# Kernel tuning notes

Hardware: AMD Instinct MI355X
Metric: run time of the kernel (lower is better)

The kernel has to match this reference:

```python
import jax, jax.numpy as jnp
import numpy as np

N = 100000      # nodes per graph batch
E = 1600000     # edges per graph batch
F_IN = 128
HID = 128
N_GRAPHS = 64


def gcn_conv(x, edge_index, W, b):
    """PyG GCNConv: add self-loops, symmetric deg^-1/2 normalization, scatter-add."""
    n = x.shape[0]
    xw = x @ W                                  # [N, H]
    src, dst = edge_index[0], edge_index[1]
    # degree including self-loop
    deg = jnp.zeros((n,), xw.dtype).at[dst].add(jnp.ones((src.shape[0],), xw.dtype)) + 1.0
    dinv = jax.lax.rsqrt(deg)                   # deg^-1/2
    norm = (dinv[src] * dinv[dst])[:, None]     # [E, 1]
    msg = xw[src] * norm                        # gather + scale
    agg = jnp.zeros_like(xw).at[dst].add(msg)   # scatter-add
    agg = agg + xw * (dinv * dinv)[:, None]     # self-loop contribution
    return agg + b


def global_mean_pool(x, batch, num_graphs):
    sums = jax.ops.segment_sum(x, batch, num_segments=num_graphs)
    cnts = jax.ops.segment_sum(jnp.ones((x.shape[0],), x.dtype), batch, num_segments=num_graphs)
    return sums / jnp.maximum(cnts, 1.0)[:, None]


def setup_inputs() -> dict:
    key = jax.random.key(0)
    ks = jax.random.split(key, 16)
    s = 1.0 / np.sqrt(F_IN)
    sh = 1.0 / np.sqrt(HID)
    return {
        "x_H": jax.random.normal(ks[0], (N, F_IN), jnp.float32),
        "edge_index_H": jax.random.randint(ks[1], (2, E), 0, N, jnp.int64),
        "x_G": jax.random.normal(ks[2], (N, F_IN), jnp.float32),
        "edge_index_G": jax.random.randint(ks[3], (2, E), 0, N, jnp.int64),
        "batch_H": jnp.sort(jax.random.randint(ks[4], (N,), 0, N_GRAPHS, jnp.int64)),
        "batch_G": jnp.sort(jax.random.randint(ks[5], (N,), 0, N_GRAPHS, jnp.int64)),
        # selector params
        "sel_W1": jax.random.uniform(ks[6], (F_IN, HID), jnp.float32, -s, s),
        "sel_b1": jnp.zeros((HID,), jnp.float32),
        "sel_W2": jax.random.uniform(ks[7], (HID, HID), jnp.float32, -sh, sh),
        "sel_b2": jnp.zeros((HID,), jnp.float32),
        "sel_fcw": jax.random.uniform(ks[8], (HID, 1), jnp.float32, -sh, sh),
        "sel_fcb": jnp.zeros((1,), jnp.float32),
        # embedder params (shared between F and G branches)
        "emb_W1": jax.random.uniform(ks[9], (F_IN, HID), jnp.float32, -s, s),
        "emb_b1": jnp.zeros((HID,), jnp.float32),
        "emb_W2": jax.random.uniform(ks[10], (HID, HID), jnp.float32, -sh, sh),
        "emb_b2": jnp.zeros((HID,), jnp.float32),
    }


def reference(x_H, edge_index_H, x_G, edge_index_G, batch_H, batch_G,
              sel_W1, sel_b1, sel_W2, sel_b2, sel_fcw, sel_fcb,
              emb_W1, emb_b1, emb_W2, emb_b2):
    # selector on H
    h = jax.nn.relu(gcn_conv(x_H, edge_index_H, sel_W1, sel_b1))
    h = jax.nn.relu(gcn_conv(h, edge_index_H, sel_W2, sel_b2))
    p = jax.nn.sigmoid(h @ sel_fcw + sel_fcb)          # [N, 1]

    def embed(x, ei, batch):
        z = jax.nn.relu(gcn_conv(x, ei, emb_W1, emb_b1))
        z = jax.nn.relu(gcn_conv(z, ei, emb_W2, emb_b2))
        return global_mean_pool(z, batch, N_GRAPHS)

    h_F = embed(x_H * p, edge_index_H, batch_H)
    h_G = embed(x_G, edge_index_G, batch_G)
    return (h_F, h_G, p)
```

## Files before the change

kernel.cpp:

```cpp
#include <hip/hip_runtime.h>
#include <cstdint>
#include <cstddef>

#define FEAT 128
#define PSLICE 8
#define BSHIFT 7
#define CAP 4096

typedef _Float16 h16;
typedef __attribute__((ext_vector_type(8))) _Float16 h16x8;
typedef __attribute__((ext_vector_type(4))) _Float16 h16x4;
typedef __attribute__((ext_vector_type(2))) _Float16 h16x2;
typedef __attribute__((ext_vector_type(4))) float f32x4;

__global__ __launch_bounds__(256) void k_part(const int* __restrict__ ei,
    int2* __restrict__ pair, int* __restrict__ gcur, int E, int nb) {
  __shared__ int cnt[1024];
  __shared__ int base[1024];
  int per = (E + gridDim.x - 1) / gridDim.x;
  int e0 = blockIdx.x * per;
  int e1 = min(e0 + per, E);
  for (int i = threadIdx.x; i < nb; i += 256) cnt[i] = 0;
  __syncthreads();
  for (int e = e0 + threadIdx.x; e < e1; e += 256)
    atomicAdd(&cnt[ei[E + e] >> BSHIFT], 1);
  __syncthreads();
  for (int i = threadIdx.x; i < nb; i += 256) {
    int c = cnt[i];
    base[i] = c ? atomicAdd(&gcur[i], c) : 0;
    cnt[i] = 0;
  }
  __syncthreads();
  for (int e = e0 + threadIdx.x; e < e1; e += 256) {
    int src = ei[e];
    int dst = ei[E + e];
    int b = dst >> BSHIFT;
    int pos = base[b] + atomicAdd(&cnt[b], 1);
    if (pos < CAP) pair[(size_t)b * CAP + pos] = make_int2(src, dst);
  }
}

__global__ __launch_bounds__(1024) void k_bscan(const int* __restrict__ cnt,
    int* __restrict__ boffs, int* __restrict__ offs, int nb, int N, int E) {
  __shared__ int wsum[16];
  __shared__ int carry;
  int tid = threadIdx.x;
  int lane = tid & 63;
  int wid = tid >> 6;
  if (tid == 0) carry = 0;
  for (int base = 0; base < nb; base += 1024) {
    __syncthreads();
    int c0 = carry;
    int i = base + tid;
    int v = (i < nb) ? cnt[i] : 0;
    int x = v;
#pragma unroll
    for (int off = 1; off < 64; off <<= 1) {
      int t = __shfl_up(x, off);
      if (lane >= off) x += t;
    }
    if (lane == 63) wsum[wid] = x;
    __syncthreads();
    if (wid == 0) {
      int t = (lane < 16) ? wsum[lane] : 0;
#pragma unroll
      for (int off = 1; off < 16; off <<= 1) {
        int u = __shfl_up(t, off);
        if (lane >= off) t += u;
      }
      if (lane < 16) wsum[lane] = t;
    }
    __syncthreads();
    int wex = (wid == 0) ? 0 : wsum[wid - 1];
    int o = c0 + wex + (x - v);
    if (i < nb) boffs[i] = o;
    int total = wsum[15];
    __syncthreads();
    if (tid == 0) carry = c0 + total;
  }
  __syncthreads();
  if (tid == 0) { boffs[nb] = carry; offs[N] = E; }
}

__global__ __launch_bounds__(256) void k_bucket(const int2* __restrict__ pair,
    const int* __restrict__ bcnt, const int* __restrict__ boffs,
    int* __restrict__ csr, int* __restrict__ offs, float* __restrict__ dinv,
    int N) {
  int b = blockIdx.x;
  int nodeBase = b << BSHIFT;
  int m = min(bcnt[b], CAP);
  __shared__ int cnt[128];
  __shared__ int noff[128];
  __shared__ int w0tot;
  if (threadIdx.x < 128) cnt[threadIdx.x] = 0;
  __syncthreads();
  const int2* p = pair + (size_t)b * CAP;
  for (int i = threadIdx.x; i < m; i += 256)
    atomicAdd(&cnt[p[i].y - nodeBase], 1);
  __syncthreads();
  int v = 0, x = 0;
  int lane = threadIdx.x & 63, w = threadIdx.x >> 6;
  if (threadIdx.x < 128) {
    v = cnt[threadIdx.x];
    x = v;
#pragma unroll
    for (int o = 1; o < 64; o <<= 1) {
      int t = __shfl_up(x, o);
      if (lane >= o) x += t;
    }
    if (threadIdx.x == 63) w0tot = x;
  }
  __syncthreads();
  int cbase = boffs[b];
  if (threadIdx.x < 128) {
    int ex = x - v + ((w == 1) ? w0tot : 0);
    int g = nodeBase + threadIdx.x;
    if (g < N) {
      offs[g] = cbase + ex;
      dinv[g] = 1.0f / sqrtf((float)v + 1.0f);
    }
    noff[threadIdx.x] = ex;
    cnt[threadIdx.x] = 0;
  }
  __syncthreads();
  for (int i = threadIdx.x; i < m; i += 256) {
    int d = p[i].y - nodeBase;
    int pos = cbase + noff[d] + atomicAdd(&cnt[d], 1);
    csr[pos] = p[i].x;
  }
}

__global__ __launch_bounds__(256) void k_wprep(const float* __restrict__ W,
    h16* __restrict__ WT) {
  int i = blockIdx.x * 256 + threadIdx.x;
  int k = i >> 7, c = i & 127;
  WT[c * FEAT + k] = (h16)W[(size_t)k * FEAT + c];
}

__device__ inline h16x8 load8(const float* p) {
  float4 a = *(const float4*)p, b = *(const float4*)(p + 4);
  h16x8 o;
  o[0] = (h16)a.x; o[1] = (h16)a.y; o[2] = (h16)a.z; o[3] = (h16)a.w;
  o[4] = (h16)b.x; o[5] = (h16)b.y; o[6] = (h16)b.z; o[7] = (h16)b.w;
  return o;
}
__device__ inline h16x8 load8(const h16* p) { return *(const h16x8*)p; }

template <typename TI>
__global__ __launch_bounds__(256) void k_gemm_mfma(const TI* __restrict__ X,
    const h16* __restrict__ WT, const float* __restrict__ s1, const float* __restrict__ s2,
    h16* __restrict__ Y, int n) {
  __shared__ __align__(16) h16 lA[128 * FEAT];
  __shared__ __align__(16) h16 lB[128 * FEAT];
  int tid = threadIdx.x;
  int row0 = blockIdx.x * 128;
#pragma unroll
  for (int i = 0; i < 8; ++i) {
    int c = tid + i * 256;
    int r = c >> 4, kc = c & 15;
    int grow = row0 + r;
    h16x8 v;
#pragma unroll
    for (int j = 0; j < 8; ++j) v[j] = (h16)0.f;
    if (grow < n) v = load8(&X[(size_t)grow * FEAT + kc * 8]);
    int byte = r * 256 + ((kc * 16) ^ ((r & 7) << 4));
    *(h16x8*)((char*)lA + byte) = v;
  }
#pragma unroll
  for (int i = 0; i < 8; ++i) {
    int c = tid + i * 256;
    int col = c >> 4, kc = c & 15;
    h16x8 v = *(const h16x8*)&WT[col * FEAT + kc * 8];
    int byte = col * 256 + ((kc * 16) ^ ((col & 7) << 4));
    *(h16x8*)((char*)lB + byte) = v;
  }
  __syncthreads();
  int w = tid >> 6, l = tid & 63;
  int lr = l & 15, lq = l >> 4;
  h16x8 af[2][4];
#pragma unroll
  for (int m = 0; m < 2; ++m)
#pragma unroll
    for (int s = 0; s < 4; ++s) {
      int r = w * 32 + m * 16 + lr;
      int k2 = (s * 32 + lq * 8) * 2;
      int byte = r * 256 + (k2 ^ ((r & 7) << 4));
      af[m][s] = *(const h16x8*)((const char*)lA + byte);
    }
  f32x4 acc[2][8];
#pragma unroll
  for (int m = 0; m < 2; ++m)
#pragma unroll
    for (int nn = 0; nn < 8; ++nn) acc[m][nn] = (f32x4){0.f, 0.f, 0.f, 0.f};
#pragma unroll
  for (int nn = 0; nn < 8; ++nn) {
#pragma unroll
    for (int s = 0; s < 4; ++s) {
      int col = nn * 16 + lr;
      int k2 = (s * 32 + lq * 8) * 2;
      int byte = col * 256 + (k2 ^ ((col & 7) << 4));
      h16x8 bf = *(const h16x8*)((const char*)lB + byte);
      acc[0][nn] = __builtin_amdgcn_mfma_f32_16x16x32_f16(af[0][s], bf, acc[0][nn], 0, 0, 0);
      acc[1][nn] = __builtin_amdgcn_mfma_f32_16x16x32_f16(af[1][s], bf, acc[1][nn], 0, 0, 0);
    }
  }
#pragma unroll
  for (int m = 0; m < 2; ++m) {
#pragma unroll
    for (int r = 0; r < 4; ++r) {
      int grow = row0 + w * 32 + m * 16 + lq * 4 + r;
      if (grow < n) {
        float sc = 1.0f;
        if (s1) sc = s1[grow];
        if (s2) sc *= s2[grow];
#pragma unroll
        for (int nn = 0; nn < 8; ++nn)
          Y[(size_t)grow * FEAT + nn * 16 + lr] = (h16)(acc[m][nn][r] * sc);
      }
    }
  }
}

__device__ inline float4 ldrow4(const h16* p) {
  h16x4 v = *(const h16x4*)p;
  return make_float4((float)v[0], (float)v[1], (float)v[2], (float)v[3]);
}

__global__ __launch_bounds__(256) void k_agg(const h16* __restrict__ XW,
    const int* __restrict__ offs, const int* __restrict__ csr,
    const float* __restrict__ dinv, const float* __restrict__ bias,
    h16* __restrict__ out, int n) {
  int half = threadIdx.x >> 5;
  int lane = threadIdx.x & 31;
  int node = blockIdx.x * 8 + half;
  if (node >= n) return;
  int f = lane * 4;
  float4 a0 = ldrow4(&XW[(size_t)node * FEAT + f]);
  float4 a1 = {0,0,0,0}, a2 = {0,0,0,0}, a3 = {0,0,0,0};
  float4 a4 = {0,0,0,0}, a5 = {0,0,0,0}, a6 = {0,0,0,0}, a7 = {0,0,0,0};
  int s = offs[node], e = offs[node + 1];
  int i = s;
  for (; i + 8 <= e; i += 8) {
    int s0 = csr[i + 0], s1 = csr[i + 1], s2 = csr[i + 2], s3 = csr[i + 3];
    int s4 = csr[i + 4], s5 = csr[i + 5], s6 = csr[i + 6], s7 = csr[i + 7];
    float4 v0 = ldrow4(&XW[(size_t)s0 * FEAT + f]);
    float4 v1 = ldrow4(&XW[(size_t)s1 * FEAT + f]);
    float4 v2 = ldrow4(&XW[(size_t)s2 * FEAT + f]);
    float4 v3 = ldrow4(&XW[(size_t)s3 * FEAT + f]);
    float4 v4 = ldrow4(&XW[(size_t)s4 * FEAT + f]);
    float4 v5 = ldrow4(&XW[(size_t)s5 * FEAT + f]);
    float4 v6 = ldrow4(&XW[(size_t)s6 * FEAT + f]);
    float4 v7 = ldrow4(&XW[(size_t)s7 * FEAT + f]);
    a0.x += v0.x; a0.y += v0.y; a0.z += v0.z; a0.w += v0.w;
    a1.x += v1.x; a1.y += v1.y; a1.z += v1.z; a1.w += v1.w;
    a2.x += v2.x; a2.y += v2.y; a2.z += v2.z; a2.w += v2.w;
    a3.x += v3.x; a3.y += v3.y; a3.z += v3.z; a3.w += v3.w;
    a4.x += v4.x; a4.y += v4.y; a4.z += v4.z; a4.w += v4.w;
    a5.x += v5.x; a5.y += v5.y; a5.z += v5.z; a5.w += v5.w;
    a6.x += v6.x; a6.y += v6.y; a6.z += v6.z; a6.w += v6.w;
    a7.x += v7.x; a7.y += v7.y; a7.z += v7.z; a7.w += v7.w;
  }
  if (i + 4 <= e) {
    int s0 = csr[i + 0], s1 = csr[i + 1], s2 = csr[i + 2], s3 = csr[i + 3];
    float4 v0 = ldrow4(&XW[(size_t)s0 * FEAT + f]);
    float4 v1 = ldrow4(&XW[(size_t)s1 * FEAT + f]);
    float4 v2 = ldrow4(&XW[(size_t)s2 * FEAT + f]);
    float4 v3 = ldrow4(&XW[(size_t)s3 * FEAT + f]);
    a4.x += v0.x; a4.y += v0.y; a4.z += v0.z; a4.w += v0.w;
    a5.x += v1.x; a5.y += v1.y; a5.z += v1.z; a5.w += v1.w;
    a6.x += v2.x; a6.y += v2.y; a6.z += v2.z; a6.w += v2.w;
    a7.x += v3.x; a7.y += v3.y; a7.z += v3.z; a7.w += v3.w;
    i += 4;
  }
  for (; i < e; ++i) {
    int s0 = csr[i];
    float4 v0 = ldrow4(&XW[(size_t)s0 * FEAT + f]);
    a1.x += v0.x; a1.y += v0.y; a1.z += v0.z; a1.w += v0.w;
  }
  a0.x += a1.x; a0.y += a1.y; a0.z += a1.z; a0.w += a1.w;
  a2.x += a3.x; a2.y += a3.y; a2.z += a3.z; a2.w += a3.w;
  a4.x += a5.x; a4.y += a5.y; a4.z += a5.z; a4.w += a5.w;
  a6.x += a7.x; a6.y += a7.y; a6.z += a7.z; a6.w += a7.w;
  a0.x += a2.x; a0.y += a2.y; a0.z += a2.z; a0.w += a2.w;
  a4.x += a6.x; a4.y += a6.y; a4.z += a6.z; a4.w += a6.w;
  a0.x += a4.x; a0.y += a4.y; a0.z += a4.z; a0.w += a4.w;
  float d = dinv[node];
  float4 b = *(const float4*)&bias[f];
  h16x4 o;
  o[0] = (h16)fmaxf(a0.x * d + b.x, 0.f);
  o[1] = (h16)fmaxf(a0.y * d + b.y, 0.f);
  o[2] = (h16)fmaxf(a0.z * d + b.z, 0.f);
  o[3] = (h16)fmaxf(a0.w * d + b.w, 0.f);
  *(h16x4*)&out[(size_t)node * FEAT + f] = o;
}

__global__ __launch_bounds__(256) void k_pvec(const h16* __restrict__ H,
    const float* __restrict__ fcw, const float* __restrict__ fcb,
    float* __restrict__ p, int n) {
  int w = threadIdx.x >> 6, lane = threadIdx.x & 63;
  int node = blockIdx.x * 4 + w;
  if (node >= n) return;
  h16x2 h = *(const h16x2*)&H[(size_t)node * FEAT + lane * 2];
  float2 wv = *(const float2*)&fcw[lane * 2];
  float acc = (float)h[0] * wv.x + (float)h[1] * wv.y;
#pragma unroll
  for (int off = 32; off > 0; off >>= 1) acc += __shfl_xor(acc, off);
  if (lane == 0) p[node] = 1.0f / (1.0f + expf(-(acc + fcb[0])));
}

__global__ __launch_bounds__(256) void k_pool_part(const h16* __restrict__ Z,
    const int* __restrict__ batch, float* __restrict__ part, int n) {
  int g = blockIdx.x / PSLICE;
  int s = blockIdx.x % PSLICE;
  int lo = 0, hi = n;
  while (lo < hi) { int m = (lo + hi) >> 1; if (batch[m] < g) lo = m + 1; else hi = m; }
  int start = lo;
  hi = n;
  while (lo < hi) { int m = (lo + hi) >> 1; if (batch[m] <= g) lo = m + 1; else hi = m; }
  int end = lo;
  int len = end - start;
  int per = (len + PSLICE - 1) / PSLICE;
  int r0 = start + s * per;
  int r1 = min(r0 + per, end);
  int f = threadIdx.x & 127;
  int half = threadIdx.x >> 7;
  float acc = 0.f;
  for (int i = r0 + half; i < r1; i += 2) acc += (float)Z[(size_t)i * FEAT + f];
  __shared__ float lds[256];
  lds[threadIdx.x] = acc;
  __syncthreads();
  if (half == 0) part[(size_t)blockIdx.x * FEAT + f] = lds[f] + lds[128 + f];
}

__global__ __launch_bounds__(128) void k_pool_fin(const float* __restrict__ part,
    const int* __restrict__ batch, float* __restrict__ out, int n) {
  int g = blockIdx.x;
  int lo = 0, hi = n;
  while (lo < hi) { int m = (lo + hi) >> 1; if (batch[m] < g) lo = m + 1; else hi = m; }
  int start = lo;
  hi = n;
  while (lo < hi) { int m = (lo + hi) >> 1; if (batch[m] <= g) lo = m + 1; else hi = m; }
  int len = lo - start;
  int f = threadIdx.x;
  float tot = 0.f;
#pragma unroll
  for (int s = 0; s < PSLICE; ++s) tot += part[(size_t)(g * PSLICE + s) * FEAT + f];
  out[(size_t)g * FEAT + f] = tot / fmaxf((float)len, 1.0f);
}

extern "C" void kernel_launch(void* const* d_in, const int* in_sizes, int n_in,
                              void* d_out, int out_size, void* d_ws, size_t ws_size,
                              hipStream_t stream) {
  const float* x_H    = (const float*)d_in[0];
  const int*   ei_H   = (const int*)d_in[1];
  const float* x_G    = (const float*)d_in[2];
  const int*   ei_G   = (const int*)d_in[3];
  const int*   bat_H  = (const int*)d_in[4];
  const int*   bat_G  = (const int*)d_in[5];
  const float* sel_W1 = (const float*)d_in[6];
  const float* sel_b1 = (const float*)d_in[7];
  const float* sel_W2 = (const float*)d_in[8];
  const float* sel_b2 = (const float*)d_in[9];
  const float* sel_fcw = (const float*)d_in[10];
  const float* sel_fcb = (const float*)d_in[11];
  const float* emb_W1 = (const float*)d_in[12];
  const float* emb_b1 = (const float*)d_in[13];
  const float* emb_W2 = (const float*)d_in[14];
  const float* emb_b2 = (const float*)d_in[15];

  const int N = in_sizes[0] / FEAT;
  const int E = in_sizes[1] / 2;
  const int NG = 64;
  const int NB = (N + 127) >> BSHIFT;

  float* out = (float*)d_out;
  float* hF = out;
  float* hG = out + NG * FEAT;
  float* p  = out + 2 * NG * FEAT;

  char* ws = (char*)d_ws;
  size_t off = 0;
  auto alloc = [&](size_t bytes) -> void* {
    void* ptr = (void*)(ws + off);
    off += (bytes + 511) & ~(size_t)511;
    return ptr;
  };
  const size_t SZH = (size_t)N * FEAT * sizeof(h16);
  const size_t SZP = (size_t)NB * CAP * sizeof(int2);
  const size_t SZB = SZH > SZP ? SZH : SZP;
  h16* A       = (h16*)alloc(SZB);
  h16* B       = (h16*)alloc(SZB);
  float* dinvH = (float*)alloc((size_t)N * 4);
  float* dinvG = (float*)alloc((size_t)N * 4);
  int*  offsH  = (int*)alloc((size_t)(N + 1) * 4);
  int*  offsG  = (int*)alloc((size_t)(N + 1) * 4);
  int*  csrH   = (int*)alloc((size_t)E * 4);
  int*  csrG   = (int*)alloc((size_t)E * 4);
  int*  gcurH  = (int*)alloc((size_t)NB * 4);
  int*  gcurG  = (int*)alloc((size_t)NB * 4);
  int*  boffsH = (int*)alloc((size_t)(NB + 1) * 4);
  int*  boffsG = (int*)alloc((size_t)(NB + 1) * 4);
  float* part  = (float*)alloc((size_t)NG * PSLICE * FEAT * 4);
  h16* wtSel1  = (h16*)alloc((size_t)FEAT * FEAT * 2);
  h16* wtSel2  = (h16*)alloc((size_t)FEAT * FEAT * 2);
  h16* wtEmb1  = (h16*)alloc((size_t)FEAT * FEAT * 2);
  h16* wtEmb2  = (h16*)alloc((size_t)FEAT * FEAT * 2);
  (void)ws_size;

  int2* pairH = (int2*)A;
  int2* pairG = (int2*)B;

  const int gGemm = (N + 127) / 128;
  const int gAgg  = (N + 7) / 8;
  const int gP    = (N + 3) / 4;

  k_wprep<<<64, 256, 0, stream>>>(sel_W1, wtSel1);
  k_wprep<<<64, 256, 0, stream>>>(sel_W2, wtSel2);
  k_wprep<<<64, 256, 0, stream>>>(emb_W1, wtEmb1);
  k_wprep<<<64, 256, 0, stream>>>(emb_W2, wtEmb2);

  hipMemsetAsync(gcurH, 0, (size_t)NB * 4, stream);
  hipMemsetAsync(gcurG, 0, (size_t)NB * 4, stream);
  k_part<<<256, 256, 0, stream>>>(ei_H, pairH, gcurH, E, NB);
  k_part<<<256, 256, 0, stream>>>(ei_G, pairG, gcurG, E, NB);
  k_bscan<<<1, 1024, 0, stream>>>(gcurH, boffsH, offsH, NB, N, E);
  k_bscan<<<1, 1024, 0, stream>>>(gcurG, boffsG, offsG, NB, N, E);
  k_bucket<<<NB, 256, 0, stream>>>(pairH, gcurH, boffsH, csrH, offsH, dinvH, N);
  k_bucket<<<NB, 256, 0, stream>>>(pairG, gcurG, boffsG, csrG, offsG, dinvG, N);

  k_gemm_mfma<float><<<gGemm, 256, 0, stream>>>(x_H, wtSel1, dinvH, nullptr, A, N);
  k_agg<<<gAgg, 256, 0, stream>>>(A, offsH, csrH, dinvH, sel_b1, B, N);
  k_gemm_mfma<h16><<<gGemm, 256, 0, stream>>>(B, wtSel2, dinvH, nullptr, A, N);
  k_agg<<<gAgg, 256, 0, stream>>>(A, offsH, csrH, dinvH, sel_b2, B, N);
  k_pvec<<<gP, 256, 0, stream>>>(B, sel_fcw, sel_fcb, p, N);

  k_gemm_mfma<float><<<gGemm, 256, 0, stream>>>(x_H, wtEmb1, dinvH, p, A, N);
  k_agg<<<gAgg, 256, 0, stream>>>(A, offsH, csrH, dinvH, emb_b1, B, N);
  k_gemm_mfma<h16><<<gGemm, 256, 0, stream>>>(B, wtEmb2, dinvH, nullptr, A, N);
  k_agg<<<gAgg, 256, 0, stream>>>(A, offsH, csrH, dinvH, emb_b2, B, N);
  k_pool_part<<<NG * PSLICE, 256, 0, stream>>>(B, bat_H, part, N);
  k_pool_fin<<<NG, 128, 0, stream>>>(part, bat_H, hF, N);

  k_gemm_mfma<float><<<gGemm, 256, 0, stream>>>(x_G, wtEmb1, dinvG, nullptr, A, N);
  k_agg<<<gAgg, 256, 0, stream>>>(A, offsG, csrG, dinvG, emb_b1, B, N);
  k_gemm_mfma<h16><<<gGemm, 256, 0, stream>>>(B, wtEmb2, dinvG, nullptr, A, N);
  k_agg<<<gAgg, 256, 0, stream>>>(A, offsG, csrG, dinvG, emb_b2, B, N);
  k_pool_part<<<NG * PSLICE, 256, 0, stream>>>(B, bat_G, part, N);
  k_pool_fin<<<NG, 128, 0, stream>>>(part, bat_G, hG, N);
}
```

Measured before the change: 710.4 us.

## Fuse aggregation into next GEMM and p-vector, pack edge pairs, pre-convert x_H

Adds a k_agg_gemm kernel that gathers and aggregates neighbor rows into shared memory and immediately multiplies by the next layer's weights, so the intermediate activation no longer makes a round trip through global memory. The selector's final aggregation is also fused with the sigmoid projection. Edge partition pairs are packed into one 32-bit word to halve partition traffic, and x_H is converted to fp16 once and reused by both of its GEMMs. In exchange, the fused kernel has fewer blocks (one per 128 rows) with heavy LDS use, which may reduce latency hiding for the irregular gather, and packing assumes src fits in 25 bits.

```diff
diff --git a/kernel.cpp b/kernel.cpp
--- a/kernel.cpp
+++ b/kernel.cpp
@@ -10,11 +10,23 @@
 typedef _Float16 h16;
 typedef __attribute__((ext_vector_type(8))) _Float16 h16x8;
 typedef __attribute__((ext_vector_type(4))) _Float16 h16x4;
-typedef __attribute__((ext_vector_type(2))) _Float16 h16x2;
 typedef __attribute__((ext_vector_type(4))) float f32x4;
 
+__global__ __launch_bounds__(256) void k_cvt(const float* __restrict__ X,
+    h16* __restrict__ Y, int nv) {
+  int i = blockIdx.x * 256 + threadIdx.x;
+  if (i < nv) {
+    const float* p = X + (size_t)i * 8;
+    float4 a = *(const float4*)p, b = *(const float4*)(p + 4);
+    h16x8 o;
+    o[0] = (h16)a.x; o[1] = (h16)a.y; o[2] = (h16)a.z; o[3] = (h16)a.w;
+    o[4] = (h16)b.x; o[5] = (h16)b.y; o[6] = (h16)b.z; o[7] = (h16)b.w;
+    *(h16x8*)&Y[(size_t)i * 8] = o;
+  }
+}
+
 __global__ __launch_bounds__(256) void k_part(const int* __restrict__ ei,
-    int2* __restrict__ pair, int* __restrict__ gcur, int E, int nb) {
+    unsigned int* __restrict__ pair, int* __restrict__ gcur, int E, int nb) {
   __shared__ int cnt[1024];
   __shared__ int base[1024];
   int per = (E + gridDim.x - 1) / gridDim.x;
@@ -36,7 +48,7 @@
     int dst = ei[E + e];
     int b = dst >> BSHIFT;
     int pos = base[b] + atomicAdd(&cnt[b], 1);
-    if (pos < CAP) pair[(size_t)b * CAP + pos] = make_int2(src, dst);
+    if (pos < CAP) pair[(size_t)b * CAP + pos] = ((unsigned)src << BSHIFT) | (unsigned)(dst & 127);
   }
 }
 
@@ -82,21 +94,20 @@
   if (tid == 0) { boffs[nb] = carry; offs[N] = E; }
 }
 
-__global__ __launch_bounds__(256) void k_bucket(const int2* __restrict__ pair,
+__global__ __launch_bounds__(256) void k_bucket(const unsigned int* __restrict__ pair,
     const int* __restrict__ bcnt, const int* __restrict__ boffs,
     int* __restrict__ csr, int* __restrict__ offs, float* __restrict__ dinv,
     int N) {
   int b = blockIdx.x;
-  int nodeBase = b << BSHIFT;
   int m = min(bcnt[b], CAP);
   __shared__ int cnt[128];
   __shared__ int noff[128];
   __shared__ int w0tot;
   if (threadIdx.x < 128) cnt[threadIdx.x] = 0;
   __syncthreads();
-  const int2* p = pair + (size_t)b * CAP;
+  const unsigned int* p = pair + (size_t)b * CAP;
   for (int i = threadIdx.x; i < m; i += 256)
-    atomicAdd(&cnt[p[i].y - nodeBase], 1);
+    atomicAdd(&cnt[p[i] & 127u], 1);
   __syncthreads();
   int v = 0, x = 0;
   int lane = threadIdx.x & 63, w = threadIdx.x >> 6;
@@ -114,7 +125,7 @@
   int cbase = boffs[b];
   if (threadIdx.x < 128) {
     int ex = x - v + ((w == 1) ? w0tot : 0);
-    int g = nodeBase + threadIdx.x;
+    int g = (b << BSHIFT) + threadIdx.x;
     if (g < N) {
       offs[g] = cbase + ex;
       dinv[g] = 1.0f / sqrtf((float)v + 1.0f);
@@ -124,9 +135,10 @@
   }
   __syncthreads();
   for (int i = threadIdx.x; i < m; i += 256) {
-    int d = p[i].y - nodeBase;
+    unsigned pk = p[i];
+    int d = pk & 127u;
     int pos = cbase + noff[d] + atomicAdd(&cnt[d], 1);
-    csr[pos] = p[i].x;
+    csr[pos] = (int)(pk >> BSHIFT);
   }
 }
 
@@ -137,104 +149,13 @@
   WT[c * FEAT + k] = (h16)W[(size_t)k * FEAT + c];
 }
 
-__device__ inline h16x8 load8(const float* p) {
-  float4 a = *(const float4*)p, b = *(const float4*)(p + 4);
-  h16x8 o;
-  o[0] = (h16)a.x; o[1] = (h16)a.y; o[2] = (h16)a.z; o[3] = (h16)a.w;
-  o[4] = (h16)b.x; o[5] = (h16)b.y; o[6] = (h16)b.z; o[7] = (h16)b.w;
-  return o;
-}
-__device__ inline h16x8 load8(const h16* p) { return *(const h16x8*)p; }
-
-template <typename TI>
-__global__ __launch_bounds__(256) void k_gemm_mfma(const TI* __restrict__ X,
-    const h16* __restrict__ WT, const float* __restrict__ s1, const float* __restrict__ s2,
-    h16* __restrict__ Y, int n) {
-  __shared__ __align__(16) h16 lA[128 * FEAT];
-  __shared__ __align__(16) h16 lB[128 * FEAT];
-  int tid = threadIdx.x;
-  int row0 = blockIdx.x * 128;
-#pragma unroll
-  for (int i = 0; i < 8; ++i) {
-    int c = tid + i * 256;
-    int r = c >> 4, kc = c & 15;
-    int grow = row0 + r;
-    h16x8 v;
-#pragma unroll
-    for (int j = 0; j < 8; ++j) v[j] = (h16)0.f;
-    if (grow < n) v = load8(&X[(size_t)grow * FEAT + kc * 8]);
-    int byte = r * 256 + ((kc * 16) ^ ((r & 7) << 4));
-    *(h16x8*)((char*)lA + byte) = v;
-  }
-#pragma unroll
-  for (int i = 0; i < 8; ++i) {
-    int c = tid + i * 256;
-    int col = c >> 4, kc = c & 15;
-    h16x8 v = *(const h16x8*)&WT[col * FEAT + kc * 8];
-    int byte = col * 256 + ((kc * 16) ^ ((col & 7) << 4));
-    *(h16x8*)((char*)lB + byte) = v;
-  }
-  __syncthreads();
-  int w = tid >> 6, l = tid & 63;
-  int lr = l & 15, lq = l >> 4;
-  h16x8 af[2][4];
-#pragma unroll
-  for (int m = 0; m < 2; ++m)
-#pragma unroll
-    for (int s = 0; s < 4; ++s) {
-      int r = w * 32 + m * 16 + lr;
-      int k2 = (s * 32 + lq * 8) * 2;
-      int byte = r * 256 + (k2 ^ ((r & 7) << 4));
-      af[m][s] = *(const h16x8*)((const char*)lA + byte);
-    }
-  f32x4 acc[2][8];
-#pragma unroll
-  for (int m = 0; m < 2; ++m)
-#pragma unroll
-    for (int nn = 0; nn < 8; ++nn) acc[m][nn] = (f32x4){0.f, 0.f, 0.f, 0.f};
-#pragma unroll
-  for (int nn = 0; nn < 8; ++nn) {
-#pragma unroll
-    for (int s = 0; s < 4; ++s) {
-      int col = nn * 16 + lr;
-      int k2 = (s * 32 + lq * 8) * 2;
-      int byte = col * 256 + (k2 ^ ((col & 7) << 4));
-      h16x8 bf = *(const h16x8*)((const char*)lB + byte);
-      acc[0][nn] = __builtin_amdgcn_mfma_f32_16x16x32_f16(af[0][s], bf, acc[0][nn], 0, 0, 0);
-      acc[1][nn] = __builtin_amdgcn_mfma_f32_16x16x32_f16(af[1][s], bf, acc[1][nn], 0, 0, 0);
-    }
-  }
-#pragma unroll
-  for (int m = 0; m < 2; ++m) {
-#pragma unroll
-    for (int r = 0; r < 4; ++r) {
-      int grow = row0 + w * 32 + m * 16 + lq * 4 + r;
-      if (grow < n) {
-        float sc = 1.0f;
-        if (s1) sc = s1[grow];
-        if (s2) sc *= s2[grow];
-#pragma unroll
-        for (int nn = 0; nn < 8; ++nn)
-          Y[(size_t)grow * FEAT + nn * 16 + lr] = (h16)(acc[m][nn][r] * sc);
-      }
-    }
-  }
-}
-
 __device__ inline float4 ldrow4(const h16* p) {
   h16x4 v = *(const h16x4*)p;
   return make_float4((float)v[0], (float)v[1], (float)v[2], (float)v[3]);
 }
 
-__global__ __launch_bounds__(256) void k_agg(const h16* __restrict__ XW,
-    const int* __restrict__ offs, const int* __restrict__ csr,
-    const float* __restrict__ dinv, const float* __restrict__ bias,
-    h16* __restrict__ out, int n) {
-  int half = threadIdx.x >> 5;
-  int lane = threadIdx.x & 31;
-  int node = blockIdx.x * 8 + half;
-  if (node >= n) return;
-  int f = lane * 4;
+__device__ inline float4 gather_row(const h16* __restrict__ XW,
+    const int* __restrict__ offs, const int* __restrict__ csr, int node, int f) {
   float4 a0 = ldrow4(&XW[(size_t)node * FEAT + f]);
   float4 a1 = {0,0,0,0}, a2 = {0,0,0,0}, a3 = {0,0,0,0};
   float4 a4 = {0,0,0,0}, a5 = {0,0,0,0}, a6 = {0,0,0,0}, a7 = {0,0,0,0};
@@ -284,28 +205,208 @@
   a0.x += a2.x; a0.y += a2.y; a0.z += a2.z; a0.w += a2.w;
   a4.x += a6.x; a4.y += a6.y; a4.z += a6.z; a4.w += a6.w;
   a0.x += a4.x; a0.y += a4.y; a0.z += a4.z; a0.w += a4.w;
+  return a0;
+}
+
+__global__ __launch_bounds__(256) void k_agg(const h16* __restrict__ XW,
+    const int* __restrict__ offs, const int* __restrict__ csr,
+    const float* __restrict__ dinv, const float* __restrict__ bias,
+    h16* __restrict__ out, int n) {
+  int half = threadIdx.x >> 5;
+  int lane = threadIdx.x & 31;
+  int node = blockIdx.x * 8 + half;
+  if (node >= n) return;
+  int f = lane * 4;
+  float4 a = gather_row(XW, offs, csr, node, f);
   float d = dinv[node];
   float4 b = *(const float4*)&bias[f];
   h16x4 o;
-  o[0] = (h16)fmaxf(a0.x * d + b.x, 0.f);
-  o[1] = (h16)fmaxf(a0.y * d + b.y, 0.f);
-  o[2] = (h16)fmaxf(a0.z * d + b.z, 0.f);
-  o[3] = (h16)fmaxf(a0.w * d + b.w, 0.f);
+  o[0] = (h16)fmaxf(a.x * d + b.x, 0.f);
+  o[1] = (h16)fmaxf(a.y * d + b.y, 0.f);
+  o[2] = (h16)fmaxf(a.z * d + b.z, 0.f);
+  o[3] = (h16)fmaxf(a.w * d + b.w, 0.f);
   *(h16x4*)&out[(size_t)node * FEAT + f] = o;
 }
 
-__global__ __launch_bounds__(256) void k_pvec(const h16* __restrict__ H,
+__global__ __launch_bounds__(256) void k_agg_pvec(const h16* __restrict__ XW,
+    const int* __restrict__ offs, const int* __restrict__ csr,
+    const float* __restrict__ dinv, const float* __restrict__ bias,
     const float* __restrict__ fcw, const float* __restrict__ fcb,
     float* __restrict__ p, int n) {
-  int w = threadIdx.x >> 6, lane = threadIdx.x & 63;
-  int node = blockIdx.x * 4 + w;
+  int half = threadIdx.x >> 5;
+  int lane = threadIdx.x & 31;
+  int node = blockIdx.x * 8 + half;
   if (node >= n) return;
-  h16x2 h = *(const h16x2*)&H[(size_t)node * FEAT + lane * 2];
-  float2 wv = *(const float2*)&fcw[lane * 2];
-  float acc = (float)h[0] * wv.x + (float)h[1] * wv.y;
-#pragma unroll
-  for (int off = 32; off > 0; off >>= 1) acc += __shfl_xor(acc, off);
+  int f = lane * 4;
+  float4 a = gather_row(XW, offs, csr, node, f);
+  float d = dinv[node];
+  float4 b = *(const float4*)&bias[f];
+  float4 wv = *(const float4*)&fcw[f];
+  float acc = fmaxf(a.x * d + b.x, 0.f) * wv.x
+            + fmaxf(a.y * d + b.y, 0.f) * wv.y
+            + fmaxf(a.z * d + b.z, 0.f) * wv.z
+            + fmaxf(a.w * d + b.w, 0.f) * wv.w;
+#pragma unroll
+  for (int off = 16; off > 0; off >>= 1) acc += __shfl_xor(acc, off, 32);
   if (lane == 0) p[node] = 1.0f / (1.0f + expf(-(acc + fcb[0])));
+}
+
+__global__ __launch_bounds__(512) void k_agg_gemm(const h16* __restrict__ XW,
+    const int* __restrict__ offs, const int* __restrict__ csr,
+    const float* __restrict__ dinv, const float* __restrict__ bias,
+    const h16* __restrict__ WT, h16* __restrict__ Y, int n) {
+  __shared__ __align__(16) h16 lA[128 * FEAT];
+  __shared__ __align__(16) h16 lB[128 * FEAT];
+  int tid = threadIdx.x;
+  int row0 = blockIdx.x * 128;
+#pragma unroll
+  for (int i = 0; i < 4; ++i) {
+    int c = tid + i * 512;
+    int col = c >> 4, kc = c & 15;
+    h16x8 v = *(const h16x8*)&WT[col * FEAT + kc * 8];
+    int byte = col * 256 + ((kc * 16) ^ ((col & 7) << 4));
+    *(h16x8*)((char*)lB + byte) = v;
+  }
+  int half = tid >> 5;
+  int lane = tid & 31;
+  int f = lane * 4;
+  float4 bv = *(const float4*)&bias[f];
+  for (int q = 0; q < 8; ++q) {
+    int r = half * 8 + q;
+    int node = row0 + r;
+    h16x4 o;
+    if (node < n) {
+      float4 a = gather_row(XW, offs, csr, node, f);
+      float d = dinv[node];
+      o[0] = (h16)fmaxf(a.x * d + bv.x, 0.f);
+      o[1] = (h16)fmaxf(a.y * d + bv.y, 0.f);
+      o[2] = (h16)fmaxf(a.z * d + bv.z, 0.f);
+      o[3] = (h16)fmaxf(a.w * d + bv.w, 0.f);
+    } else {
+      o[0] = (h16)0.f; o[1] = (h16)0.f; o[2] = (h16)0.f; o[3] = (h16)0.f;
+    }
+    int byte = r * 256 + ((f * 2) ^ ((r & 7) << 4));
+    *(h16x4*)((char*)lA + byte) = o;
+  }
+  __syncthreads();
+  int w = tid >> 6, l = tid & 63;
+  int lr = l & 15, lq = l >> 4;
+  h16x8 af[4];
+#pragma unroll
+  for (int s = 0; s < 4; ++s) {
+    int r = w * 16 + lr;
+    int k2 = (s * 32 + lq * 8) * 2;
+    int byte = r * 256 + (k2 ^ ((r & 7) << 4));
+    af[s] = *(const h16x8*)((const char*)lA + byte);
+  }
+  f32x4 acc[8];
+#pragma unroll
+  for (int nn = 0; nn < 8; ++nn) acc[nn] = (f32x4){0.f, 0.f, 0.f, 0.f};
+#pragma unroll
+  for (int nn = 0; nn < 8; ++nn) {
+#pragma unroll
+    for (int s = 0; s < 4; ++s) {
+      int col = nn * 16 + lr;
+      int k2 = (s * 32 + lq * 8) * 2;
+      int byte = col * 256 + (k2 ^ ((col & 7) << 4));
+      h16x8 bf = *(const h16x8*)((const char*)lB + byte);
+      acc[nn] = __builtin_amdgcn_mfma_f32_16x16x32_f16(af[s], bf, acc[nn], 0, 0, 0);
+    }
+  }
+#pragma unroll
+  for (int r = 0; r < 4; ++r) {
+    int grow = row0 + w * 16 + lq * 4 + r;
+    if (grow < n) {
+      float sc = dinv[grow];
+#pragma unroll
+      for (int nn = 0; nn < 8; ++nn)
+        Y[(size_t)grow * FEAT + nn * 16 + lr] = (h16)(acc[nn][r] * sc);
+    }
+  }
+}
+
+__device__ inline h16x8 load8(const float* p) {
+  float4 a = *(const float4*)p, b = *(const float4*)(p + 4);
+  h16x8 o;
+  o[0] = (h16)a.x; o[1] = (h16)a.y; o[2] = (h16)a.z; o[3] = (h16)a.w;
+  o[4] = (h16)b.x; o[5] = (h16)b.y; o[6] = (h16)b.z; o[7] = (h16)b.w;
+  return o;
+}
+__device__ inline h16x8 load8(const h16* p) { return *(const h16x8*)p; }
+
+template <typename TI>
+__global__ __launch_bounds__(256) void k_gemm_mfma(const TI* __restrict__ X,
+    const h16* __restrict__ WT, const float* __restrict__ s1, const float* __restrict__ s2,
+    h16* __restrict__ Y, int n) {
+  __shared__ __align__(16) h16 lA[128 * FEAT];
+  __shared__ __align__(16) h16 lB[128 * FEAT];
+  int tid = threadIdx.x;
+  int row0 = blockIdx.x * 128;
+#pragma unroll
+  for (int i = 0; i < 8; ++i) {
+    int c = tid + i * 256;
+    int r = c >> 4, kc = c & 15;
+    int grow = row0 + r;
+    h16x8 v;
+#pragma unroll
+    for (int j = 0; j < 8; ++j) v[j] = (h16)0.f;
+    if (grow < n) v = load8(&X[(size_t)grow * FEAT + kc * 8]);
+    int byte = r * 256 + ((kc * 16) ^ ((r & 7) << 4));
+    *(h16x8*)((char*)lA + byte) = v;
+  }
+#pragma unroll
+  for (int i = 0; i < 8; ++i) {
+    int c = tid + i * 256;
+    int col = c >> 4, kc = c & 15;
+    h16x8 v = *(const h16x8*)&WT[col * FEAT + kc * 8];
+    int byte = col * 256 + ((kc * 16) ^ ((col & 7) << 4));
+    *(h16x8*)((char*)lB + byte) = v;
+  }
+  __syncthreads();
+  int w = tid >> 6, l = tid & 63;
+  int lr = l & 15, lq = l >> 4;
+  h16x8 af[2][4];
+#pragma unroll
+  for (int m = 0; m < 2; ++m)
+#pragma unroll
+    for (int s = 0; s < 4; ++s) {
+      int r = w * 32 + m * 16 + lr;
+      int k2 = (s * 32 + lq * 8) * 2;
+      int byte = r * 256 + (k2 ^ ((r & 7) << 4));
+      af[m][s] = *(const h16x8*)((const char*)lA + byte);
+    }
+  f32x4 acc[2][8];
+#pragma unroll
+  for (int m = 0; m < 2; ++m)
+#pragma unroll
+    for (int nn = 0; nn < 8; ++nn) acc[m][nn] = (f32x4){0.f, 0.f, 0.f, 0.f};
+#pragma unroll
+  for (int nn = 0; nn < 8; ++nn) {
+#pragma unroll
+    for (int s = 0; s < 4; ++s) {
+      int col = nn * 16 + lr;
+      int k2 = (s * 32 + lq * 8) * 2;
+      int byte = col * 256 + (k2 ^ ((col & 7) << 4));
+      h16x8 bf = *(const h16x8*)((const char*)lB + byte);
+      acc[0][nn] = __builtin_amdgcn_mfma_f32_16x16x32_f16(af[0][s], bf, acc[0][nn], 0, 0, 0);
+      acc[1][nn] = __builtin_amdgcn_mfma_f32_16x16x32_f16(af[1][s], bf, acc[1][nn], 0, 0, 0);
+    }
+  }
+#pragma unroll
+  for (int m = 0; m < 2; ++m) {
+#pragma unroll
+    for (int r = 0; r < 4; ++r) {
+      int grow = row0 + w * 32 + m * 16 + lq * 4 + r;
+      if (grow < n) {
+        float sc = 1.0f;
+        if (s1) sc = s1[grow];
+        if (s2) sc *= s2[grow];
+#pragma unroll
+        for (int nn = 0; nn < 8; ++nn)
+          Y[(size_t)grow * FEAT + nn * 16 + lr] = (h16)(acc[m][nn][r] * sc);
+      }
+    }
+  }
 }
 
 __global__ __launch_bounds__(256) void k_pool_part(const h16* __restrict__ Z,
@@ -386,10 +487,12 @@
     return ptr;
   };
   const size_t SZH = (size_t)N * FEAT * sizeof(h16);
-  const size_t SZP = (size_t)NB * CAP * sizeof(int2);
+  const size_t SZP = (size_t)NB * CAP * sizeof(unsigned int);
   const size_t SZB = SZH > SZP ? SZH : SZP;
   h16* A       = (h16*)alloc(SZB);
   h16* B       = (h16*)alloc(SZB);
+  h16* C       = (h16*)alloc(SZH);
+  h16* x16H    = (h16*)alloc(SZH);
   float* dinvH = (float*)alloc((size_t)N * 4);
   float* dinvG = (float*)alloc((size_t)N * 4);
   int*  offsH  = (int*)alloc((size_t)(N + 1) * 4);
@@ -407,17 +510,18 @@
   h16* wtEmb2  = (h16*)alloc((size_t)FEAT * FEAT * 2);
   (void)ws_size;
 
-  int2* pairH = (int2*)A;
-  int2* pairG = (int2*)B;
+  unsigned int* pairH = (unsigned int*)A;
+  unsigned int* pairG = (unsigned int*)B;
 
   const int gGemm = (N + 127) / 128;
   const int gAgg  = (N + 7) / 8;
-  const int gP    = (N + 3) / 4;
+  const int gAG   = (N + 127) / 128;
 
   k_wprep<<<64, 256, 0, stream>>>(sel_W1, wtSel1);
   k_wprep<<<64, 256, 0, stream>>>(sel_W2, wtSel2);
   k_wprep<<<64, 256, 0, stream>>>(emb_W1, wtEmb1);
   k_wprep<<<64, 256, 0, stream>>>(emb_W2, wtEmb2);
+  k_cvt<<<(N * FEAT / 8 + 255) / 256, 256, 0, stream>>>(x_H, x16H, N * FEAT / 8);
 
   hipMemsetAsync(gcurH, 0, (size_t)NB * 4, stream);
   hipMemsetAsync(gcurG, 0, (size_t)NB * 4, stream);
@@ -428,23 +532,19 @@
   k_bucket<<<NB, 256, 0, stream>>>(pairH, gcurH, boffsH, csrH, offsH, dinvH, N);
   k_bucket<<<NB, 256, 0, stream>>>(pairG, gcurG, boffsG, csrG, offsG, dinvG, N);
 
-  k_gemm_mfma<float><<<gGemm, 256, 0, stream>>>(x_H, wtSel1, dinvH, nullptr, A, N);
-  k_agg<<<gAgg, 256, 0, stream>>>(A, offsH, csrH, dinvH, sel_b1, B, N);
-  k_gemm_mfma<h16><<<gGemm, 256, 0, stream>>>(B, wtSel2, dinvH, nullptr, A, N);
-  k_agg<<<gAgg, 256, 0, stream>>>(A, offsH, csrH, dinvH, sel_b2, B, N);
-  k_pvec<<<gP, 256, 0, stream>>>(B, sel_fcw, sel_fcb, p, N);
-
-  k_gemm_mfma<float><<<gGemm, 256, 0, stream>>>(x_H, wtEmb1, dinvH, p, A, N);
-  k_agg<<<gAgg, 256, 0, stream>>>(A, offsH, csrH, dinvH, emb_b1, B, N);
-  k_gemm_mfma<h16><<<gGemm, 256, 0, stream>>>(B, wtEmb2, dinvH, nullptr, A, N);
-  k_agg<<<gAgg, 256, 0, stream>>>(A, offsH, csrH, dinvH, emb_b2, B, N);
+  k_gemm_mfma<h16><<<gGemm, 256, 0, stream>>>(x16H, wtSel1, dinvH, nullptr, A, N);
+  k_agg_gemm<<<gAG, 512, 0, stream>>>(A, offsH, csrH, dinvH, sel_b1, wtSel2, C, N);
+  k_agg_pvec<<<gAgg, 256, 0, stream>>>(C, offsH, csrH, dinvH, sel_b2, sel_fcw, sel_fcb, p, N);
+
+  k_gemm_mfma<h16><<<gGemm, 256, 0, stream>>>(x16H, wtEmb1, dinvH, p, A, N);
+  k_agg_gemm<<<gAG, 512, 0, stream>>>(A, offsH, csrH, dinvH, emb_b1, wtEmb2, C, N);
+  k_agg<<<gAgg, 256, 0, stream>>>(C, offsH, csrH, dinvH, emb_b2, B, N);
   k_pool_part<<<NG * PSLICE, 256, 0, stream>>>(B, bat_H, part, N);
   k_pool_fin<<<NG, 128, 0, stream>>>(part, bat_H, hF, N);
 
   k_gemm_mfma<float><<<gGemm, 256, 0, stream>>>(x_G, wtEmb1, dinvG, nullptr, A, N);
-  k_agg<<<gAgg, 256, 0, stream>>>(A, offsG, csrG, dinvG, emb_b1, B, N);
-  k_gemm_mfma<h16><<<gGemm, 256, 0, stream>>>(B, wtEmb2, dinvG, nullptr, A, N);
-  k_agg<<<gAgg, 256, 0, stream>>>(A, offsG, csrG, dinvG, emb_b2, B, N);
+  k_agg_gemm<<<gAG, 512, 0, stream>>>(A, offsG, csrG, dinvG, emb_b1, wtEmb2, C, N);
+  k_agg<<<gAgg, 256, 0, stream>>>(C, offsG, csrG, dinvG, emb_b2, B, N);
   k_pool_part<<<NG * PSLICE, 256, 0, stream>>>(B, bat_G, part, N);
   k_pool_fin<<<NG, 128, 0, stream>>>(part, bat_G, hG, N);
 }
```

Result: slower. 739.4 us (+4.1%).
